# Kernel tuning notes

Measured on AMD Instinct MI355X. Metric: run time of the kernel, lower is better.

The kernel has to match this reference:

```python
import jax, jax.numpy as jnp
import numpy as np

B, H, W, DIM, NH, WS, SS = 32, 56, 56, 512, 16, 7, 3
L = H * W
HD = DIM // NH
N = WS * WS
SCALE = HD ** -0.5
EPS = 1e-5


def _rel_pos_index():
    coords = np.stack(np.meshgrid(np.arange(WS), np.arange(WS), indexing='ij'))  # (2,ws,ws)
    cf = coords.reshape(2, -1)
    rc = (cf[:, :, None] - cf[:, None, :]).transpose(1, 2, 0).astype(np.int64)  # (N,N,2)
    rc[..., 0] += WS - 1
    rc[..., 1] += WS - 1
    rc[..., 0] *= 2 * WS - 1
    return rc.sum(-1)  # (N,N)


def _shift_mask():
    img = np.zeros((H, W), np.float32)
    cnt = 0
    for hs in (slice(0, -WS), slice(-WS, -SS), slice(-SS, None)):
        for ws_ in (slice(0, -WS), slice(-WS, -SS), slice(-SS, None)):
            img[hs, ws_] = cnt
            cnt += 1
    m = img.reshape(H // WS, WS, W // WS, WS).transpose(0, 2, 1, 3).reshape(-1, N)  # (nW,N)
    diff = m[:, None, :] - m[:, :, None]
    return np.where(diff != 0, -100.0, 0.0).astype(np.float32)  # (nW,N,N)


REL_IDX = jnp.asarray(_rel_pos_index())
ATTN_MASK = jnp.asarray(_shift_mask())


def _ln(x, g, b):
    mu = jnp.mean(x, -1, keepdims=True)
    var = jnp.var(x, -1, keepdims=True)
    return (x - mu) * jax.lax.rsqrt(var + EPS) * g + b


def setup_inputs() -> dict:
    key = jax.random.key(0)
    ks = jax.random.split(key, 8)
    s = 0.02
    return {
        'x': jax.random.normal(ks[0], (B, L, DIM), jnp.float32),
        'norm1_g': jnp.ones((DIM,), jnp.float32),
        'norm1_b': jnp.zeros((DIM,), jnp.float32),
        'qkv_w': jax.random.normal(ks[1], (DIM, 3 * DIM), jnp.float32) * s,
        'qkv_b': jnp.zeros((3 * DIM,), jnp.float32),
        'rel_bias_table': jax.random.normal(ks[2], ((2 * WS - 1) ** 2, NH), jnp.float32) * s,
        'proj_w': jax.random.normal(ks[3], (DIM, DIM), jnp.float32) * s,
        'proj_b': jnp.zeros((DIM,), jnp.float32),
        'norm2_g': jnp.ones((DIM,), jnp.float32),
        'norm2_b': jnp.zeros((DIM,), jnp.float32),
        'fc1_w': jax.random.normal(ks[4], (DIM, 4 * DIM), jnp.float32) * s,
        'fc1_b': jnp.zeros((4 * DIM,), jnp.float32),
        'fc2_w': jax.random.normal(ks[5], (4 * DIM, DIM), jnp.float32) * s,
        'fc2_b': jnp.zeros((DIM,), jnp.float32),
    }


def reference(x, norm1_g, norm1_b, qkv_w, qkv_b, rel_bias_table, proj_w, proj_b,
              norm2_g, norm2_b, fc1_w, fc1_b, fc2_w, fc2_b):
    shortcut = x
    h = _ln(x, norm1_g, norm1_b).reshape(B, H, W, DIM)
    # cyclic shift
    h = jnp.roll(h, (-SS, -SS), axis=(1, 2))
    # window partition -> (B*nW, N, C)
    nWh, nWw = H // WS, W // WS
    h = h.reshape(B, nWh, WS, nWw, WS, DIM).transpose(0, 1, 3, 2, 4, 5).reshape(-1, N, DIM)
    Bw = h.shape[0]
    # qkv
    qkv = (h @ qkv_w + qkv_b).reshape(Bw, N, 3, NH, HD).transpose(2, 0, 3, 1, 4)
    q, k, v = qkv[0], qkv[1], qkv[2]  # (Bw, NH, N, HD)
    attn = jnp.einsum('bhnd,bhmd->bhnm', q * SCALE, k)
    # relative position bias (NH, N, N)
    bias = rel_bias_table[REL_IDX.reshape(-1)].reshape(N, N, NH).transpose(2, 0, 1)
    attn = attn + bias[None]
    # shift mask: (B, nW, NH, N, N) + (1, nW, 1, N, N)
    nW = nWh * nWw
    attn = attn.reshape(B, nW, NH, N, N) + ATTN_MASK[None, :, None]
    attn = jax.nn.softmax(attn.reshape(Bw, NH, N, N), axis=-1)
    out = jnp.einsum('bhnm,bhmd->bhnd', attn, v).transpose(0, 2, 1, 3).reshape(Bw, N, DIM)
    out = out @ proj_w + proj_b
    # window reverse + reverse shift
    out = out.reshape(B, nWh, nWw, WS, WS, DIM).transpose(0, 1, 3, 2, 4, 5).reshape(B, H, W, DIM)
    out = jnp.roll(out, (SS, SS), axis=(1, 2)).reshape(B, L, DIM)
    x = shortcut + out
    # MLP (GELU exact, matching torch nn.GELU default)
    y = _ln(x, norm2_g, norm2_b)
    y = jax.nn.gelu(y @ fc1_w + fc1_b, approximate=False) @ fc2_w + fc2_b
    return x + y
```

## Files before the change

kernel.cpp:

```cpp
#include <hip/hip_runtime.h>
#include <hip/hip_bf16.h>
#include <math.h>

#define MROWS 100352
#define MHALF 50176
#define DIM   512
#define LL    3136
#define HH    56
#define NHEAD 16
#define NWIN  49
#define SSH   3
#define SCALE_QK 0.17677669529663687f

typedef __bf16 bf16;
typedef __bf16 bf16x8 __attribute__((ext_vector_type(8)));
typedef float  f32x4  __attribute__((ext_vector_type(4)));

typedef __attribute__((address_space(1))) void* gas_ptr;
typedef __attribute__((address_space(3))) void* las_ptr;

__device__ __forceinline__ void gload_lds16(const void* g, void* l) {
  __builtin_amdgcn_global_load_lds((gas_ptr)g, (las_ptr)l, 16, 0, 0);
}

__device__ __forceinline__ int nat_row(int r) {
  int bw = r / 49;
  int n  = r - bw * 49;
  int b  = bw >> 6;
  int wh = (bw >> 3) & 7;
  int ww = bw & 7;
  int i  = n / 7;
  int j  = n - i * 7;
  int hs = wh * 7 + i + SSH; if (hs >= HH) hs -= HH;
  int ws = ww * 7 + j + SSH; if (ws >= HH) ws -= HH;
  return b * LL + hs * HH + ws;
}

__global__ __launch_bounds__(256) void tcast_kernel(const float* __restrict__ src,
                                                    bf16* __restrict__ dst,
                                                    int Kd, int Nd) {
  __shared__ float t[32][33];
  int tx = threadIdx.x & 31, ty = threadIdx.x >> 5;
  int n0 = blockIdx.x * 32, k0 = blockIdx.y * 32;
  #pragma unroll
  for (int yy = ty; yy < 32; yy += 8)
    t[yy][tx] = src[(size_t)(k0 + yy) * Nd + n0 + tx];
  __syncthreads();
  #pragma unroll
  for (int yy = ty; yy < 32; yy += 8)
    dst[(size_t)(n0 + yy) * Kd + k0 + tx] = (bf16)t[tx][yy];
}

template<int PERM>
__global__ __launch_bounds__(256) void ln_kernel(const float* __restrict__ x,
                                                 const float* __restrict__ gw,
                                                 const float* __restrict__ bw_,
                                                 bf16* __restrict__ out) {
  int wave = threadIdx.x >> 6, lane = threadIdx.x & 63;
  int r = blockIdx.x * 4 + wave;
  int src = PERM ? nat_row(r) : r;
  const float* px = x + (size_t)src * DIM + lane * 8;
  float4 v0 = *(const float4*)px;
  float4 v1 = *(const float4*)(px + 4);
  float s = v0.x + v0.y + v0.z + v0.w + v1.x + v1.y + v1.z + v1.w;
  float q = v0.x*v0.x + v0.y*v0.y + v0.z*v0.z + v0.w*v0.w
          + v1.x*v1.x + v1.y*v1.y + v1.z*v1.z + v1.w*v1.w;
  #pragma unroll
  for (int m = 1; m < 64; m <<= 1) { s += __shfl_xor(s, m); q += __shfl_xor(q, m); }
  float mean = s * (1.f / DIM);
  float var  = q * (1.f / DIM) - mean * mean;
  float rstd = rsqrtf(var + 1e-5f);
  int c0 = lane * 8;
  float4 g0 = *(const float4*)(gw + c0),  g1 = *(const float4*)(gw + c0 + 4);
  float4 b0 = *(const float4*)(bw_ + c0), b1 = *(const float4*)(bw_ + c0 + 4);
  bf16x8 o;
  o[0] = (bf16)((v0.x - mean) * rstd * g0.x + b0.x);
  o[1] = (bf16)((v0.y - mean) * rstd * g0.y + b0.y);
  o[2] = (bf16)((v0.z - mean) * rstd * g0.z + b0.z);
  o[3] = (bf16)((v0.w - mean) * rstd * g0.w + b0.w);
  o[4] = (bf16)((v1.x - mean) * rstd * g1.x + b1.x);
  o[5] = (bf16)((v1.y - mean) * rstd * g1.y + b1.y);
  o[6] = (bf16)((v1.z - mean) * rstd * g1.z + b1.z);
  o[7] = (bf16)((v1.w - mean) * rstd * g1.w + b1.w);
  *(bf16x8*)(out + (size_t)r * DIM + c0) = o;
}

template<int MODE, int KD, int ND>
__global__ __launch_bounds__(256) void gemm_kernel(const bf16* __restrict__ A,
                                                   const bf16* __restrict__ Bt,
                                                   const float* __restrict__ bias,
                                                   const float* __restrict__ resid,
                                                   bf16* __restrict__ outB,
                                                   float* __restrict__ outF) {
  __shared__ bf16 As[128 * 32];
  __shared__ bf16 Bs[128 * 32];
  int tid = threadIdx.x;
  int wv = tid >> 6, lane = tid & 63;
  int lr = lane & 15, lg = lane >> 4;
  int wr = wv >> 1, wc = wv & 1;
  int tm = blockIdx.y, tn = blockIdx.x;
  const int arow0 = tm * 128;
  const int brow0 = tn * 128;
  int srow = lane >> 2;
  int scol = (lane & 3) * 8;

  f32x4 zero4 = {0.f, 0.f, 0.f, 0.f};
  f32x4 acc[4][4];
  #pragma unroll
  for (int i = 0; i < 4; i++)
    #pragma unroll
    for (int j = 0; j < 4; j++) acc[i][j] = zero4;

  for (int kt = 0; kt < KD / 32; ++kt) {
    #pragma unroll
    for (int q2 = 0; q2 < 2; ++q2) {
      int rbase = (wv * 2 + q2) * 16;
      const bf16* ga = A + (size_t)(arow0 + rbase + srow) * KD + kt * 32 + scol;
      gload_lds16(ga, As + rbase * 32);
      const bf16* gb = Bt + (size_t)(brow0 + rbase + srow) * KD + kt * 32 + scol;
      gload_lds16(gb, Bs + rbase * 32);
    }
    __syncthreads();
    bf16x8 af[4], bfr[4];
    #pragma unroll
    for (int mi = 0; mi < 4; mi++)
      af[mi] = *(const bf16x8*)(As + (wr * 64 + mi * 16 + lr) * 32 + lg * 8);
    #pragma unroll
    for (int ni = 0; ni < 4; ni++)
      bfr[ni] = *(const bf16x8*)(Bs + (wc * 64 + ni * 16 + lr) * 32 + lg * 8);
    #pragma unroll
    for (int mi = 0; mi < 4; mi++)
      #pragma unroll
      for (int ni = 0; ni < 4; ni++)
        acc[mi][ni] = __builtin_amdgcn_mfma_f32_16x16x32_bf16(af[mi], bfr[ni], acc[mi][ni], 0, 0, 0);
    __syncthreads();
  }

  #pragma unroll
  for (int mi = 0; mi < 4; mi++) {
    #pragma unroll
    for (int rr = 0; rr < 4; rr++) {
      int row = arow0 + wr * 64 + mi * 16 + lg * 4 + rr;
      int orow = (MODE == 1) ? nat_row(row) : row;
      #pragma unroll
      for (int ni = 0; ni < 4; ni++) {
        int col = brow0 + wc * 64 + ni * 16 + lr;
        float v = acc[mi][ni][rr] + bias[col];
        if (MODE == 0) {
          outB[(size_t)row * ND + col] = (bf16)v;
        } else if (MODE == 1) {
          outF[(size_t)orow * ND + col] = resid[(size_t)orow * ND + col] + v;
        } else if (MODE == 2) {
          float g = 0.5f * v * (1.f + erff(v * 0.70710678118654752f));
          outB[(size_t)row * ND + col] = (bf16)g;
        } else {
          outF[(size_t)row * ND + col] = resid[(size_t)row * ND + col] + v;
        }
      }
    }
  }
}

__global__ __launch_bounds__(256) void attn_kernel(const bf16* __restrict__ qkv,
                                                   const float* __restrict__ table,
                                                   bf16* __restrict__ attnO) {
  __shared__ bf16 P[4][64 * 72];
  int wave = threadIdx.x >> 6, lane = threadIdx.x & 63;
  int lr = lane & 15, lg = lane >> 4;
  int wid = blockIdx.x * 4 + wave;
  int win = wid >> 4, head = wid & 15;
  int wh = (win >> 3) & 7, ww = win & 7;
  const bf16* base = qkv + (size_t)win * (49 * 1536) + head * 32;

  f32x4 zero4 = {0.f, 0.f, 0.f, 0.f};
  bf16x8 aq[4], bk[4];
  #pragma unroll
  for (int mi = 0; mi < 4; mi++) {
    int q = mi * 16 + lr; if (q > 48) q = 48;
    aq[mi] = *(const bf16x8*)(base + q * 1536 + lg * 8);
    bk[mi] = *(const bf16x8*)(base + 512 + q * 1536 + lg * 8);
  }
  f32x4 sacc[4][4];
  #pragma unroll
  for (int mi = 0; mi < 4; mi++)
    #pragma unroll
    for (int ni = 0; ni < 4; ni++)
      sacc[mi][ni] = __builtin_amdgcn_mfma_f32_16x16x32_bf16(aq[mi], bk[ni], zero4, 0, 0, 0);

  float rsum[4][4];
  #pragma unroll
  for (int mi = 0; mi < 4; mi++) {
    #pragma unroll
    for (int rr = 0; rr < 4; rr++) {
      int qrow = mi * 16 + lg * 4 + rr;
      int qc = qrow > 48 ? 48 : qrow;
      int i1 = qc / 7, j1 = qc - i1 * 7;
      int labq = ((wh < 7) ? 0 : ((i1 < 4) ? 1 : 2)) * 3 + ((ww < 7) ? 0 : ((j1 < 4) ? 1 : 2));
      float pv[4];
      float mv = -3.0e30f;
      #pragma unroll
      for (int ni = 0; ni < 4; ni++) {
        int key = ni * 16 + lr;
        float v;
        if (key > 48) {
          v = -1e30f;
        } else {
          int i2 = key / 7, j2 = key - i2 * 7;
          int labk = ((wh < 7) ? 0 : ((i2 < 4) ? 1 : 2)) * 3 + ((ww < 7) ? 0 : ((j2 < 4) ? 1 : 2));
          int idx = (i1 - i2 + 6) * 13 + (j1 - j2 + 6);
          float msk = (labq == labk) ? 0.f : -100.f;
          v = sacc[mi][ni][rr] * SCALE_QK + table[idx * 16 + head] + msk;
        }
        pv[ni] = v;
        mv = fmaxf(mv, v);
      }
      #pragma unroll
      for (int m = 1; m < 16; m <<= 1) mv = fmaxf(mv, __shfl_xor(mv, m));
      float sum = 0.f;
      #pragma unroll
      for (int ni = 0; ni < 4; ni++) {
        float p = __expf(pv[ni] - mv);
        sum += p;
        P[wave][qrow * 72 + ni * 16 + lr] = (bf16)p;
      }
      #pragma unroll
      for (int m = 1; m < 16; m <<= 1) sum += __shfl_xor(sum, m);
      rsum[mi][rr] = sum;
    }
  }
  __syncthreads();

  f32x4 oacc[4][2];
  #pragma unroll
  for (int mi = 0; mi < 4; mi++) { oacc[mi][0] = zero4; oacc[mi][1] = zero4; }
  #pragma unroll
  for (int ks = 0; ks < 2; ks++) {
    bf16x8 bv[2];
    #pragma unroll
    for (int n2 = 0; n2 < 2; n2++) {
      #pragma unroll
      for (int j = 0; j < 8; j++) {
        int kv = ks * 32 + lg * 8 + j; if (kv > 48) kv = 48;
        bv[n2][j] = base[1024 + (size_t)kv * 1536 + n2 * 16 + lr];
      }
    }
    #pragma unroll
    for (int mi = 0; mi < 4; mi++) {
      bf16x8 ap = *(const bf16x8*)(&P[wave][(mi * 16 + lr) * 72 + ks * 32 + lg * 8]);
      #pragma unroll
      for (int n2 = 0; n2 < 2; n2++)
        oacc[mi][n2] = __builtin_amdgcn_mfma_f32_16x16x32_bf16(ap, bv[n2], oacc[mi][n2], 0, 0, 0);
    }
  }
  #pragma unroll
  for (int mi = 0; mi < 4; mi++) {
    #pragma unroll
    for (int rr = 0; rr < 4; rr++) {
      int qrow = mi * 16 + lg * 4 + rr;
      if (qrow < 49) {
        float inv = 1.f / rsum[mi][rr];
        #pragma unroll
        for (int n2 = 0; n2 < 2; n2++)
          attnO[((size_t)win * 49 + qrow) * DIM + head * 32 + n2 * 16 + lr] =
              (bf16)(oacc[mi][n2][rr] * inv);
      }
    }
  }
}

extern "C" void kernel_launch(void* const* d_in, const int* in_sizes, int n_in,
                              void* d_out, int out_size, void* d_ws, size_t ws_size,
                              hipStream_t stream) {
  const float* x      = (const float*)d_in[0];
  const float* n1g    = (const float*)d_in[1];
  const float* n1b    = (const float*)d_in[2];
  const float* qkv_w  = (const float*)d_in[3];
  const float* qkv_b  = (const float*)d_in[4];
  const float* tabl   = (const float*)d_in[5];
  const float* proj_w = (const float*)d_in[6];
  const float* proj_b = (const float*)d_in[7];
  const float* n2g    = (const float*)d_in[8];
  const float* n2b    = (const float*)d_in[9];
  const float* fc1_w  = (const float*)d_in[10];
  const float* fc1_b  = (const float*)d_in[11];
  const float* fc2_w  = (const float*)d_in[12];
  const float* fc2_b  = (const float*)d_in[13];
  float* out = (float*)d_out;

  char* ws = (char*)d_ws;
  bf16*  RegA   = (bf16*)ws;
  bf16*  RegB   = (bf16*)(ws + 102760448);
  float* x2     = (float*)(ws + 102760448 + 308281344);
  bf16*  qkvWt  = (bf16*)(ws + 102760448 + 308281344 + 205520896);
  bf16*  projWt = qkvWt + 1536 * 512;
  bf16*  fc1Wt  = projWt + 512 * 512;
  bf16*  fc2Wt  = fc1Wt + 2048 * 512;

  tcast_kernel<<<dim3(1536 / 32, 512 / 32), 256, 0, stream>>>(qkv_w, qkvWt, 512, 1536);
  tcast_kernel<<<dim3(512 / 32, 512 / 32), 256, 0, stream>>>(proj_w, projWt, 512, 512);
  tcast_kernel<<<dim3(2048 / 32, 512 / 32), 256, 0, stream>>>(fc1_w, fc1Wt, 512, 2048);
  tcast_kernel<<<dim3(512 / 32, 2048 / 32), 256, 0, stream>>>(fc2_w, fc2Wt, 2048, 512);

  ln_kernel<1><<<MROWS / 4, 256, 0, stream>>>(x, n1g, n1b, RegA);
  gemm_kernel<0, 512, 1536><<<dim3(12, MROWS / 128), 256, 0, stream>>>(
      RegA, qkvWt, qkv_b, nullptr, RegB, nullptr);
  attn_kernel<<<2048 * 16 / 4, 256, 0, stream>>>(RegB, tabl, RegA);
  gemm_kernel<1, 512, 512><<<dim3(4, MROWS / 128), 256, 0, stream>>>(
      RegA, projWt, proj_b, x, nullptr, x2);
  ln_kernel<0><<<MROWS / 4, 256, 0, stream>>>(x2, n2g, n2b, RegA);
  for (int c = 0; c < 2; ++c) {
    const bf16* a1 = RegA + (size_t)c * MHALF * 512;
    gemm_kernel<2, 512, 2048><<<dim3(16, MHALF / 128), 256, 0, stream>>>(
        a1, fc1Wt, fc1_b, nullptr, RegB, nullptr);
    gemm_kernel<3, 2048, 512><<<dim3(4, MHALF / 128), 256, 0, stream>>>(
        RegB, fc2Wt, fc2_b, x2 + (size_t)c * MHALF * 512, nullptr,
        out + (size_t)c * MHALF * 512);
  }
}
```

Baseline: 1.912 ms.

## Replace GEMM with 256x256-tile, 8-wave, double-buffered LDS pipelined kernel

Swaps the simple 128x128 single-buffered GEMM for a 256x256-tile kernel using 512 threads. It double-buffers K=64 chunks in LDS and issues async global-to-LDS loads interleaved with four MFMA phases, using s_setprio and explicit waitcnt/barriers. It also adds XCD-aware workgroup remapping and an XOR-swizzled LDS layout to reduce bank conflicts. The aim is to raise MFMA utilisation and hide memory latency, at the cost of 128 KB of LDS per block and fragile hand-written synchronisation.

```diff
diff --git a/kernel.cpp b/kernel.cpp
--- a/kernel.cpp
+++ b/kernel.cpp
@@ -7,8 +7,6 @@
 #define DIM   512
 #define LL    3136
 #define HH    56
-#define NHEAD 16
-#define NWIN  49
 #define SSH   3
 #define SCALE_QK 0.17677669529663687f
 
@@ -85,67 +83,133 @@
   *(bf16x8*)(out + (size_t)r * DIM + c0) = o;
 }
 
+
+#define MF(a,b,c) __builtin_amdgcn_mfma_f32_16x16x32_bf16((a),(b),(c),0,0,0)
+#define BAR() __builtin_amdgcn_s_barrier()
+#define WLG() asm volatile("s_waitcnt lgkmcnt(0)" ::: "memory")
+#define WVM(n) asm volatile("s_waitcnt vmcnt(" #n ")" ::: "memory")
+
 template<int MODE, int KD, int ND>
-__global__ __launch_bounds__(256) void gemm_kernel(const bf16* __restrict__ A,
-                                                   const bf16* __restrict__ Bt,
-                                                   const float* __restrict__ bias,
-                                                   const float* __restrict__ resid,
-                                                   bf16* __restrict__ outB,
-                                                   float* __restrict__ outF) {
-  __shared__ bf16 As[128 * 32];
-  __shared__ bf16 Bs[128 * 32];
-  int tid = threadIdx.x;
-  int wv = tid >> 6, lane = tid & 63;
-  int lr = lane & 15, lg = lane >> 4;
-  int wr = wv >> 1, wc = wv & 1;
-  int tm = blockIdx.y, tn = blockIdx.x;
-  const int arow0 = tm * 128;
-  const int brow0 = tn * 128;
-  int srow = lane >> 2;
-  int scol = (lane & 3) * 8;
-
-  f32x4 zero4 = {0.f, 0.f, 0.f, 0.f};
-  f32x4 acc[4][4];
-  #pragma unroll
-  for (int i = 0; i < 4; i++)
-    #pragma unroll
-    for (int j = 0; j < 4; j++) acc[i][j] = zero4;
-
-  for (int kt = 0; kt < KD / 32; ++kt) {
-    #pragma unroll
-    for (int q2 = 0; q2 < 2; ++q2) {
-      int rbase = (wv * 2 + q2) * 16;
-      const bf16* ga = A + (size_t)(arow0 + rbase + srow) * KD + kt * 32 + scol;
-      gload_lds16(ga, As + rbase * 32);
-      const bf16* gb = Bt + (size_t)(brow0 + rbase + srow) * KD + kt * 32 + scol;
-      gload_lds16(gb, Bs + rbase * 32);
-    }
-    __syncthreads();
-    bf16x8 af[4], bfr[4];
-    #pragma unroll
-    for (int mi = 0; mi < 4; mi++)
-      af[mi] = *(const bf16x8*)(As + (wr * 64 + mi * 16 + lr) * 32 + lg * 8);
-    #pragma unroll
-    for (int ni = 0; ni < 4; ni++)
-      bfr[ni] = *(const bf16x8*)(Bs + (wc * 64 + ni * 16 + lr) * 32 + lg * 8);
-    #pragma unroll
-    for (int mi = 0; mi < 4; mi++)
-      #pragma unroll
-      for (int ni = 0; ni < 4; ni++)
-        acc[mi][ni] = __builtin_amdgcn_mfma_f32_16x16x32_bf16(af[mi], bfr[ni], acc[mi][ni], 0, 0, 0);
-    __syncthreads();
-  }
-
-  #pragma unroll
-  for (int mi = 0; mi < 4; mi++) {
+__global__ __launch_bounds__(512, 2) void gemm256_kernel(const bf16* __restrict__ A,
+                                                         const bf16* __restrict__ Bt,
+                                                         const float* __restrict__ bias,
+                                                         const float* __restrict__ resid,
+                                                         bf16* __restrict__ outB,
+                                                         float* __restrict__ outF) {
+  constexpr int NTN = ND / 256;
+  constexpr int NI  = KD / 128;
+  __shared__ bf16 lds[65536];
+
+  const int tid = threadIdx.x, lane = tid & 63, wv = tid >> 6;
+  const int lr = lane & 15, lg = lane >> 4;
+  const int wm = wv >> 2, wn = wv & 3;
+
+  int nwg = gridDim.x, orig = blockIdx.x;
+  int q = nwg >> 3, r = nwg & 7, xcd = orig & 7;
+  int wgid = (xcd < r ? xcd * (q + 1) : r * (q + 1) + (xcd - r) * q) + (orig >> 3);
+  int tm = wgid / NTN, tn = wgid % NTN;
+
+  const bf16* gA = A  + (size_t)tm * 256 * KD;
+  const bf16* gB = Bt + (size_t)tn * 256 * KD;
+
+  const int klg  = (lg * 8) ^ ((lr & 8) ? 16 : 0);
+  const int a_rd = (wm * 128 + lr) * 32 + klg;
+  const int b_rd = (wn * 64 + lr) * 32 + klg;
+
+  const int kbOffE = (wv >> 2) * 8192;
+  const int kGlob  = (wv >> 2) * 32 + (((lane & 3) * 8) ^ ((lane & 32) ? 16 : 0));
+  const int rl0    = ((wv * 2) & 7) * 16 + (lane >> 2);
+  const int rl1    = rl0 + 16;
+  const int c0off  = ((wv * 2) & 7) * 512;
+
+#define STG(GP, DB, h, koff) \
+  gload_lds16((GP) + (size_t)((h) * 128 + rl0) * KD + (koff) + kGlob, \
+              (void*)(lds + (DB) + kbOffE + (h) * 4096 + c0off)); \
+  gload_lds16((GP) + (size_t)((h) * 128 + rl1) * KD + (koff) + kGlob, \
+              (void*)(lds + (DB) + kbOffE + (h) * 4096 + c0off + 512));
+
+  f32x4 acc[8][4];
+  #pragma unroll
+  for (int i = 0; i < 8; i++)
+    #pragma unroll
+    for (int j = 0; j < 4; j++) { acc[i][j][0]=0.f; acc[i][j][1]=0.f; acc[i][j][2]=0.f; acc[i][j][3]=0.f; }
+
+  bf16x8 Af[4][2], Bf0[2][2], Bf1[2][2];
+
+  STG(gA, 0,     0, 0)  STG(gA, 0,     1, 0)
+  STG(gB, 16384, 0, 0)  STG(gB, 16384, 1, 0)
+  STG(gA, 32768, 0, 64) STG(gA, 32768, 1, 64)
+  STG(gB, 49152, 0, 64) STG(gB, 49152, 1, 64)
+  WVM(8); BAR();
+
+#define PHASES(AB, BB, DOST, KST, ENDW) { \
+     \
+    _Pragma("unroll") for (int m = 0; m < 4; m++) { \
+      Af[m][0] = *(const bf16x8*)(lds + (AB) + m * 512 + a_rd); \
+      Af[m][1] = *(const bf16x8*)(lds + (AB) + 8192 + m * 512 + a_rd); } \
+    _Pragma("unroll") for (int n = 0; n < 2; n++) { \
+      Bf0[n][0] = *(const bf16x8*)(lds + (BB) + n * 512 + b_rd); \
+      Bf0[n][1] = *(const bf16x8*)(lds + (BB) + 8192 + n * 512 + b_rd); } \
+    BAR(); WLG(); __builtin_amdgcn_s_setprio(1); \
+    _Pragma("unroll") for (int m = 0; m < 4; m++) \
+      _Pragma("unroll") for (int n = 0; n < 2; n++) { \
+        acc[m][n] = MF(Af[m][0], Bf0[n][0], acc[m][n]); \
+        acc[m][n] = MF(Af[m][1], Bf0[n][1], acc[m][n]); } \
+    __builtin_amdgcn_s_setprio(0); BAR(); \
+     \
+    _Pragma("unroll") for (int n = 0; n < 2; n++) { \
+      Bf1[n][0] = *(const bf16x8*)(lds + (BB) + (n + 2) * 512 + b_rd); \
+      Bf1[n][1] = *(const bf16x8*)(lds + (BB) + 8192 + (n + 2) * 512 + b_rd); } \
+    if (DOST) { STG(gB, (BB), 0, (KST)) } \
+    BAR(); WLG(); __builtin_amdgcn_s_setprio(1); \
+    _Pragma("unroll") for (int m = 0; m < 4; m++) \
+      _Pragma("unroll") for (int n = 0; n < 2; n++) { \
+        acc[m][n + 2] = MF(Af[m][0], Bf1[n][0], acc[m][n + 2]); \
+        acc[m][n + 2] = MF(Af[m][1], Bf1[n][1], acc[m][n + 2]); } \
+    __builtin_amdgcn_s_setprio(0); BAR(); \
+     \
+    _Pragma("unroll") for (int m = 0; m < 4; m++) { \
+      Af[m][0] = *(const bf16x8*)(lds + (AB) + (m + 4) * 512 + a_rd); \
+      Af[m][1] = *(const bf16x8*)(lds + (AB) + 8192 + (m + 4) * 512 + a_rd); } \
+    if (DOST) { STG(gB, (BB), 1, (KST)) STG(gA, (AB), 0, (KST)) } \
+    BAR(); WLG(); __builtin_amdgcn_s_setprio(1); \
+    _Pragma("unroll") for (int m = 0; m < 4; m++) \
+      _Pragma("unroll") for (int n = 0; n < 2; n++) { \
+        acc[m + 4][n + 2] = MF(Af[m][0], Bf1[n][0], acc[m + 4][n + 2]); \
+        acc[m + 4][n + 2] = MF(Af[m][1], Bf1[n][1], acc[m + 4][n + 2]); } \
+    __builtin_amdgcn_s_setprio(0); BAR(); \
+     \
+    if (DOST) { STG(gA, (AB), 1, (KST)) } \
+    BAR(); WLG(); __builtin_amdgcn_s_setprio(1); \
+    _Pragma("unroll") for (int m = 0; m < 4; m++) \
+      _Pragma("unroll") for (int n = 0; n < 2; n++) { \
+        acc[m + 4][n] = MF(Af[m][0], Bf0[n][0], acc[m + 4][n]); \
+        acc[m + 4][n] = MF(Af[m][1], Bf0[n][1], acc[m + 4][n]); } \
+    __builtin_amdgcn_s_setprio(0); ENDW; BAR(); \
+  }
+
+  #pragma unroll 1
+  for (int I = 0; I < NI - 1; ++I) {
+    int ke = (2 * I + 2) * 64;
+    PHASES(0,     16384, 1, ke,      WVM(6));
+    PHASES(32768, 49152, 1, ke + 64, WVM(6));
+  }
+  PHASES(0,     16384, 0, 0, WVM(0));
+  PHASES(32768, 49152, 0, 0, ((void)0));
+
+#undef PHASES
+#undef STG
+
+  #pragma unroll
+  for (int fm = 0; fm < 8; fm++) {
     #pragma unroll
     for (int rr = 0; rr < 4; rr++) {
-      int row = arow0 + wr * 64 + mi * 16 + lg * 4 + rr;
+      int row = tm * 256 + wm * 128 + fm * 16 + lg * 4 + rr;
       int orow = (MODE == 1) ? nat_row(row) : row;
       #pragma unroll
-      for (int ni = 0; ni < 4; ni++) {
-        int col = brow0 + wc * 64 + ni * 16 + lr;
-        float v = acc[mi][ni][rr] + bias[col];
+      for (int fn = 0; fn < 4; fn++) {
+        int col = tn * 256 + wn * 64 + fn * 16 + lr;
+        float v = acc[fm][fn][rr] + bias[col];
         if (MODE == 0) {
           outB[(size_t)row * ND + col] = (bf16)v;
         } else if (MODE == 1) {
@@ -176,9 +240,9 @@
   bf16x8 aq[4], bk[4];
   #pragma unroll
   for (int mi = 0; mi < 4; mi++) {
-    int q = mi * 16 + lr; if (q > 48) q = 48;
-    aq[mi] = *(const bf16x8*)(base + q * 1536 + lg * 8);
-    bk[mi] = *(const bf16x8*)(base + 512 + q * 1536 + lg * 8);
+    int qq = mi * 16 + lr; if (qq > 48) qq = 48;
+    aq[mi] = *(const bf16x8*)(base + qq * 1536 + lg * 8);
+    bk[mi] = *(const bf16x8*)(base + 512 + qq * 1536 + lg * 8);
   }
   f32x4 sacc[4][4];
   #pragma unroll
@@ -302,17 +366,17 @@
   tcast_kernel<<<dim3(512 / 32, 2048 / 32), 256, 0, stream>>>(fc2_w, fc2Wt, 2048, 512);
 
   ln_kernel<1><<<MROWS / 4, 256, 0, stream>>>(x, n1g, n1b, RegA);
-  gemm_kernel<0, 512, 1536><<<dim3(12, MROWS / 128), 256, 0, stream>>>(
+  gemm256_kernel<0, 512, 1536><<<(MROWS / 256) * 6, 512, 0, stream>>>(
       RegA, qkvWt, qkv_b, nullptr, RegB, nullptr);
   attn_kernel<<<2048 * 16 / 4, 256, 0, stream>>>(RegB, tabl, RegA);
-  gemm_kernel<1, 512, 512><<<dim3(4, MROWS / 128), 256, 0, stream>>>(
+  gemm256_kernel<1, 512, 512><<<(MROWS / 256) * 2, 512, 0, stream>>>(
       RegA, projWt, proj_b, x, nullptr, x2);
   ln_kernel<0><<<MROWS / 4, 256, 0, stream>>>(x2, n2g, n2b, RegA);
   for (int c = 0; c < 2; ++c) {
     const bf16* a1 = RegA + (size_t)c * MHALF * 512;
-    gemm_kernel<2, 512, 2048><<<dim3(16, MHALF / 128), 256, 0, stream>>>(
+    gemm256_kernel<2, 512, 2048><<<(MHALF / 256) * 8, 512, 0, stream>>>(
         a1, fc1Wt, fc1_b, nullptr, RegB, nullptr);
-    gemm_kernel<3, 2048, 512><<<dim3(4, MHALF / 128), 256, 0, stream>>>(
+    gemm256_kernel<3, 2048, 512><<<(MHALF / 256) * 2, 512, 0, stream>>>(
         RegB, fc2Wt, fc2_b, x2 + (size_t)c * MHALF * 512, nullptr,
         out + (size_t)c * MHALF * 512);
   }
```

Measured after the change: 1.704 ms. 1.12x faster.
